# Kernel tuning notes

Hardware: AMD Instinct MI355X
Metric: run time of the kernel (lower is better)

Reference implementation:

```python
import jax, jax.numpy as jnp
import numpy as np

N_NODES = 100000
N_EDGES = 3200000
D_IN = 256
HID = 256
N_CLASSES = 40


def setup_inputs() -> dict:
    key = jax.random.key(0)
    k1, k2, k3, k4 = jax.random.split(key, 4)
    x = jax.random.normal(k1, (N_NODES, D_IN), dtype=jnp.float32)
    edge_index = jax.random.randint(k2, (2, N_EDGES), 0, N_NODES, dtype=jnp.int64)
    W1 = jax.random.normal(k3, (D_IN, HID), dtype=jnp.float32) * (1.0 / np.sqrt(D_IN))
    b1 = jnp.zeros((HID,), dtype=jnp.float32)
    W2 = jax.random.normal(k4, (HID, N_CLASSES), dtype=jnp.float32) * (1.0 / np.sqrt(HID))
    b2 = jnp.zeros((N_CLASSES,), dtype=jnp.float32)
    return {"x": x, "edge_index": edge_index, "W1": W1, "b1": b1, "W2": W2, "b2": b2}


def reference(x, edge_index, W1, b1, W2, b2):
    N = x.shape[0]
    loops = jnp.arange(N, dtype=edge_index.dtype)
    # gcn_norm: add self-loops, symmetric normalization D^-1/2 (A+I) D^-1/2
    src = jnp.concatenate([edge_index[0], loops])  # [E+N]
    dst = jnp.concatenate([edge_index[1], loops])
    ew = jnp.ones(src.shape[0], dtype=x.dtype)
    deg = jax.ops.segment_sum(ew, dst, num_segments=N)  # degree at target nodes
    dinv = jnp.where(deg > 0, jax.lax.rsqrt(deg), 0.0).astype(x.dtype)
    norm = dinv[src] * dinv[dst]  # [E+N]

    def propagate(h):
        # out[dst] += norm * h[src]  (SpMM via gather + segment scatter-add)
        return jax.ops.segment_sum(norm[:, None] * h[src], dst, num_segments=N)

    h = propagate(x) @ W1 + b1   # SGConv k=1 + Linear
    h = jax.nn.relu(h)
    h = propagate(h) @ W2 + b2
    return jax.nn.log_softmax(h, axis=1)
```

## Files before the change

kernel.cpp:

```cpp
#include <hip/hip_runtime.h>
#include <hip/hip_bf16.h>

#define N_NODES 100000
#define N_EDGES 3200000
#define D_IN 256
#define HID 256
#define NC 40
#define NBUCK 391
#define CHUNK 8192
#define BIN1_BLOCKS ((N_EDGES + CHUNK - 1) / CHUNK)
#define BCAP 16384
#define NPADE (NBUCK * BCAP)

typedef unsigned short u16;
typedef unsigned int u32;
typedef __attribute__((ext_vector_type(8))) short bf16x8;
typedef __attribute__((ext_vector_type(4))) float f32x4;
typedef __attribute__((ext_vector_type(2))) float f32x2;

static __device__ __forceinline__ float bf2f(u16 u) {
  union { unsigned int i; float f; } c; c.i = ((unsigned int)u) << 16; return c.f;
}
static __device__ __forceinline__ u16 f2bf(float f) {
  union { float f; unsigned int i; } c; c.f = f;
  unsigned int x = c.i;
  x += 0x7fffu + ((x >> 16) & 1u);
  return (u16)(x >> 16);
}

__global__ void k_zero(int* __restrict__ gcur) {
  int i = blockIdx.x * 256 + threadIdx.x;
  if (i < NBUCK) gcur[i] = i * BCAP;
}

__global__ __launch_bounds__(256) void k_bin1(const int* __restrict__ ei,
    int* __restrict__ gcur, u32* __restrict__ binned) {
  __shared__ int cnt[NBUCK];
  __shared__ int base[NBUCK];
  int t = threadIdx.x;
  int e0 = blockIdx.x * CHUNK;
  for (int j = t; j < NBUCK; j += 256) cnt[j] = 0;
  __syncthreads();
  for (int j = 0; j < CHUNK / 256; ++j) {
    int e = e0 + j * 256 + t;
    if (e < N_EDGES) {
      unsigned d = (unsigned)ei[N_EDGES + e];
      if (d < N_NODES) atomicAdd(&cnt[d >> 8], 1);
    }
  }
  __syncthreads();
  for (int j = t; j < NBUCK; j += 256)
    base[j] = cnt[j] ? atomicAdd(&gcur[j], cnt[j]) : 0;
  __syncthreads();
  for (int j = 0; j < CHUNK / 256; ++j) {
    int e = e0 + j * 256 + t;
    if (e < N_EDGES) {
      unsigned s = (unsigned)ei[e];
      unsigned d = (unsigned)ei[N_EDGES + e];
      if (s < N_NODES && d < N_NODES) {
        int b = d >> 8;
        int pos = atomicAdd(&base[b], 1);
        if ((unsigned)pos < NPADE)
          binned[pos] = ((d & 255u) << 17) | s;
      }
    }
  }
}

__global__ __launch_bounds__(256) void k_bin2(const u32* __restrict__ binned,
    const int* __restrict__ gcur, int* __restrict__ rp, int* __restrict__ re,
    float* __restrict__ dinv, int* __restrict__ ed) {
  __shared__ int cnt[256];
  __shared__ int s[256];
  __shared__ int cur[256];
  int b = blockIdx.x, t = threadIdx.x;
  int start = b * BCAP, end = gcur[b];
  cnt[t] = 0;
  __syncthreads();
  for (int i = start + t; i < end; i += 256)
    atomicAdd(&cnt[binned[i] >> 17], 1);
  __syncthreads();
  int v = cnt[t];
  s[t] = v;
  __syncthreads();
  for (int off = 1; off < 256; off <<= 1) {
    int add = (t >= off) ? s[t - off] : 0;
    __syncthreads();
    s[t] += add;
    __syncthreads();
  }
  int excl = s[t] - v;
  int n = b * 256 + t;
  if (n < N_NODES) {
    rp[n] = start + excl;
    re[n] = start + excl + v;
    dinv[n] = rsqrtf((float)v + 1.0f);
  }
  cur[t] = start + excl;
  __syncthreads();
  for (int i = start + t; i < end; i += 256) {
    u32 rec = binned[i];
    int pos = atomicAdd(&cur[rec >> 17], 1);
    if ((unsigned)pos < NPADE) ed[pos] = (int)(rec & 0x1FFFFu);
  }
}

__global__ void k_w1t(const float* __restrict__ W1, u16* __restrict__ w1t) {
  int n = blockIdx.x, k = threadIdx.x;
  w1t[n * 256 + k] = f2bf(W1[k * 256 + n]);
}
__global__ void k_w2t(const float* __restrict__ W2, u16* __restrict__ w2t) {
  int n = blockIdx.x, k = threadIdx.x;
  w2t[n * 256 + k] = (n < NC) ? f2bf(W2[k * NC + n]) : (u16)0;
}

__global__ __launch_bounds__(256) void k_gemm1(const float* __restrict__ x,
    const u16* __restrict__ w1t, const float* __restrict__ dinv,
    unsigned char* __restrict__ y) {
  __shared__ char smem[20480];
  short* sA = (short*)smem;
  short* sB = (short*)(smem + 10240);
  float* sdinv = (float*)(smem + 18432);
  int tid = threadIdx.x;
  int wave = tid >> 6, lane = tid & 63;
  int lq = lane >> 4, lr = lane & 15;
  int wm = (wave >> 1) * 64, wn = (wave & 1) * 64;
  int row0 = blockIdx.y * 128;
  int col0 = blockIdx.x * 128;
  int sr = tid >> 1;
  int sh = (tid & 1) * 16;
  int arow = row0 + sr;
  bool aval = arow < N_NODES;
  const float* axf = x + (size_t)arow * 256 + sh;
  const u16* bx = w1t + (size_t)(col0 + sr) * 256 + sh;
  f32x4 acc[4][4] = {};
  for (int k0 = 0; k0 < 256; k0 += 32) {
    float4 f0 = {}, f1 = {}, f2 = {}, f3 = {};
    if (aval) {
      f0 = *(const float4*)(axf + k0);
      f1 = *(const float4*)(axf + k0 + 4);
      f2 = *(const float4*)(axf + k0 + 8);
      f3 = *(const float4*)(axf + k0 + 12);
    }
    uint4 vb0 = *(const uint4*)(bx + k0);
    uint4 vb1 = *(const uint4*)(bx + k0 + 8);
    uint4 pa0, pa1;
    pa0.x = (u32)f2bf(f0.x) | ((u32)f2bf(f0.y) << 16);
    pa0.y = (u32)f2bf(f0.z) | ((u32)f2bf(f0.w) << 16);
    pa0.z = (u32)f2bf(f1.x) | ((u32)f2bf(f1.y) << 16);
    pa0.w = (u32)f2bf(f1.z) | ((u32)f2bf(f1.w) << 16);
    pa1.x = (u32)f2bf(f2.x) | ((u32)f2bf(f2.y) << 16);
    pa1.y = (u32)f2bf(f2.z) | ((u32)f2bf(f2.w) << 16);
    pa1.z = (u32)f2bf(f3.x) | ((u32)f2bf(f3.y) << 16);
    pa1.w = (u32)f2bf(f3.z) | ((u32)f2bf(f3.w) << 16);
    __syncthreads();
    *(uint4*)&sA[sr * 40 + sh] = pa0;
    *(uint4*)&sA[sr * 40 + sh + 8] = pa1;
    *(uint4*)&sB[sr * 40 + sh] = vb0;
    *(uint4*)&sB[sr * 40 + sh + 8] = vb1;
    __syncthreads();
    bf16x8 af[4], bfr[4];
#pragma unroll
    for (int mt = 0; mt < 4; ++mt)
      af[mt] = *(const bf16x8*)&sA[(wm + mt * 16 + lr) * 40 + lq * 8];
#pragma unroll
    for (int nt = 0; nt < 4; ++nt)
      bfr[nt] = *(const bf16x8*)&sB[(wn + nt * 16 + lr) * 40 + lq * 8];
#pragma unroll
    for (int mt = 0; mt < 4; ++mt)
#pragma unroll
      for (int nt = 0; nt < 4; ++nt)
        acc[mt][nt] = __builtin_amdgcn_mfma_f32_16x16x32_bf16(
            af[mt], bfr[nt], acc[mt][nt], 0, 0, 0);
  }
  __syncthreads();
  if (tid < 128) {
    int rr = row0 + tid;
    sdinv[tid] = (rr < N_NODES) ? dinv[rr] : 0.f;
  }
  __syncthreads();
#pragma unroll
  for (int mt = 0; mt < 4; ++mt)
#pragma unroll
    for (int nt = 0; nt < 4; ++nt) {
      int c = wn + nt * 16 + lr;
#pragma unroll
      for (int i = 0; i < 4; ++i) {
        int r = wm + mt * 16 + lq * 4 + i;
        float sv = sdinv[r] * acc[mt][nt][i];
        int pk = __builtin_amdgcn_cvt_pk_fp8_f32(sv, sv, 0, false);
        smem[r * 144 + c] = (char)(pk & 0xFF);
      }
    }
  __syncthreads();
  if (aval) {
    unsigned char* dst = y + (size_t)arow * 256 + col0 + (tid & 1) * 64;
    const char* srcp = smem + sr * 144 + (tid & 1) * 64;
#pragma unroll
    for (int j = 0; j < 4; ++j)
      ((uint4*)dst)[j] = *(const uint4*)(srcp + j * 16);
  }
}

#define ACC8(U) do { \
    acc[0] += __builtin_amdgcn_cvt_pk_f32_fp8((U).x, false); \
    acc[1] += __builtin_amdgcn_cvt_pk_f32_fp8((U).x, true);  \
    acc[2] += __builtin_amdgcn_cvt_pk_f32_fp8((U).y, false); \
    acc[3] += __builtin_amdgcn_cvt_pk_f32_fp8((U).y, true);  \
    acc[4] += __builtin_amdgcn_cvt_pk_f32_fp8((U).z, false); \
    acc[5] += __builtin_amdgcn_cvt_pk_f32_fp8((U).z, true);  \
    acc[6] += __builtin_amdgcn_cvt_pk_f32_fp8((U).w, false); \
    acc[7] += __builtin_amdgcn_cvt_pk_f32_fp8((U).w, true);  \
  } while (0)

__global__ __launch_bounds__(256) void k_spmm1(const uint4* __restrict__ y16,
    const int* __restrict__ ed, const int* __restrict__ rp,
    const int* __restrict__ re, const float* __restrict__ dinv,
    const float* __restrict__ b1, u16* __restrict__ h1) {
  int lane = threadIdx.x & 63;
  int row = (blockIdx.x << 2) + (threadIdx.x >> 6);
  int g = lane >> 4, p = lane & 15;
  float di = dinv[row];
  uint4 sv = y16[(size_t)row * 16 + p];
  f32x2 acc[8];
  f32x2 z2 = {0.f, 0.f};
  if (g == 0) {
    acc[0] = __builtin_amdgcn_cvt_pk_f32_fp8(sv.x, false);
    acc[1] = __builtin_amdgcn_cvt_pk_f32_fp8(sv.x, true);
    acc[2] = __builtin_amdgcn_cvt_pk_f32_fp8(sv.y, false);
    acc[3] = __builtin_amdgcn_cvt_pk_f32_fp8(sv.y, true);
    acc[4] = __builtin_amdgcn_cvt_pk_f32_fp8(sv.z, false);
    acc[5] = __builtin_amdgcn_cvt_pk_f32_fp8(sv.z, true);
    acc[6] = __builtin_amdgcn_cvt_pk_f32_fp8(sv.w, false);
    acc[7] = __builtin_amdgcn_cvt_pk_f32_fp8(sv.w, true);
  } else {
#pragma unroll
    for (int i = 0; i < 8; ++i) acc[i] = z2;
  }
  int e = rp[row], e1 = re[row];
  for (; e + 8 <= e1; e += 8) {
    int s0 = ed[e + g];
    int s1 = ed[e + 4 + g];
    uint4 u0 = y16[(size_t)s0 * 16 + p];
    uint4 u1 = y16[(size_t)s1 * 16 + p];
    ACC8(u0);
    ACC8(u1);
  }
  for (; e + 4 <= e1; e += 4) {
    int s0 = ed[e + g];
    uint4 u0 = y16[(size_t)s0 * 16 + p];
    ACC8(u0);
  }
  int rem = e1 - e;
  if (rem > 0) {
    int s0 = ed[e + (g < rem ? g : 0)];
    uint4 u0 = y16[(size_t)s0 * 16 + p];
    if (g < rem) ACC8(u0);
  }
#pragma unroll
  for (int i = 0; i < 8; ++i) {
    acc[i].x += __shfl_xor(acc[i].x, 16);
    acc[i].y += __shfl_xor(acc[i].y, 16);
    acc[i].x += __shfl_xor(acc[i].x, 32);
    acc[i].y += __shfl_xor(acc[i].y, 32);
  }
  if (g == 0) {
    const float4* bb4 = (const float4*)(b1 + p * 16);
    u16 o[16];
#pragma unroll
    for (int i = 0; i < 4; ++i) {
      float4 bb = bb4[i];
      float a0 = fmaxf(di * acc[2 * i].x + bb.x, 0.f);
      float a1 = fmaxf(di * acc[2 * i].y + bb.y, 0.f);
      float a2 = fmaxf(di * acc[2 * i + 1].x + bb.z, 0.f);
      float a3 = fmaxf(di * acc[2 * i + 1].y + bb.w, 0.f);
      o[4 * i + 0] = f2bf(a0);
      o[4 * i + 1] = f2bf(a1);
      o[4 * i + 2] = f2bf(a2);
      o[4 * i + 3] = f2bf(a3);
    }
    u16* dst = h1 + (size_t)row * HID + p * 16;
    *(uint4*)dst = *(const uint4*)&o[0];
    *(uint4*)(dst + 8) = *(const uint4*)&o[8];
  }
}

__global__ __launch_bounds__(256) void k_gemm2(const u16* __restrict__ h1,
    const u16* __restrict__ w2t, const float* __restrict__ dinv,
    u16* __restrict__ zb) {
  __shared__ char smem[16384];
  short* sA = (short*)smem;
  short* sB = (short*)(smem + 10240);
  float* sdinv = (float*)(smem + 14336);
  u16* sC = (u16*)smem;
  int tid = threadIdx.x;
  int wave = tid >> 6, lane = tid & 63;
  int lq = lane >> 4, lr = lane & 15;
  int wm = wave * 32;
  int row0 = blockIdx.x * 128;
  int sr = tid >> 1;
  int sh = (tid & 1) * 16;
  int arow = row0 + sr;
  bool aval = arow < N_NODES;
  const u16* ax = h1 + (size_t)arow * 256 + sh;
  int br = tid >> 1;
  const u16* bx = w2t + (size_t)br * 256 + sh;
  if (tid < 128) {
    int rr = row0 + tid;
    sdinv[tid] = (rr < N_NODES) ? dinv[rr] : 0.f;
  }
  f32x4 acc[2][3] = {};
  for (int k0 = 0; k0 < 256; k0 += 32) {
    uint4 a0 = {}, a1 = {};
    if (aval) {
      a0 = *(const uint4*)(ax + k0);
      a1 = *(const uint4*)(ax + k0 + 8);
    }
    uint4 b0 = {}, b1v = {};
    if (tid < 96) {
      b0 = *(const uint4*)(bx + k0);
      b1v = *(const uint4*)(bx + k0 + 8);
    }
    __syncthreads();
    *(uint4*)&sA[sr * 40 + sh] = a0;
    *(uint4*)&sA[sr * 40 + sh + 8] = a1;
    if (tid < 96) {
      *(uint4*)&sB[br * 40 + sh] = b0;
      *(uint4*)&sB[br * 40 + sh + 8] = b1v;
    }
    __syncthreads();
    bf16x8 af[2], bfr[3];
#pragma unroll
    for (int mt = 0; mt < 2; ++mt)
      af[mt] = *(const bf16x8*)&sA[(wm + mt * 16 + lr) * 40 + lq * 8];
#pragma unroll
    for (int nt = 0; nt < 3; ++nt)
      bfr[nt] = *(const bf16x8*)&sB[(nt * 16 + lr) * 40 + lq * 8];
#pragma unroll
    for (int mt = 0; mt < 2; ++mt)
#pragma unroll
      for (int nt = 0; nt < 3; ++nt)
        acc[mt][nt] = __builtin_amdgcn_mfma_f32_16x16x32_bf16(
            af[mt], bfr[nt], acc[mt][nt], 0, 0, 0);
  }
  __syncthreads();
#pragma unroll
  for (int mt = 0; mt < 2; ++mt)
#pragma unroll
    for (int nt = 0; nt < 3; ++nt) {
      int c = nt * 16 + lr;
#pragma unroll
      for (int i = 0; i < 4; ++i) {
        int r = wm + mt * 16 + lq * 4 + i;
        sC[r * 56 + c] = f2bf(sdinv[r] * acc[mt][nt][i]);
      }
    }
  __syncthreads();
  if (tid < 128) {
    int orow = row0 + tid;
    if (orow < N_NODES) {
      u16* dst = zb + (size_t)orow * NC;
#pragma unroll
      for (int j = 0; j < 5; ++j)
        ((uint4*)dst)[j] = *(const uint4*)&sC[tid * 56 + j * 8];
    }
  }
}

__global__ __launch_bounds__(256) void k_spmm2(const u16* __restrict__ zb,
    const int* __restrict__ ed, const int* __restrict__ rp,
    const int* __restrict__ re, const float* __restrict__ dinv,
    const float* __restrict__ b2, float* __restrict__ out) {
  int lane = threadIdx.x & 63;
  int row = (blockIdx.x << 2) + (threadIdx.x >> 6);
  int col = (lane < NC) ? lane : 0;
  float di = dinv[row];
  float acc = bf2f(zb[(size_t)row * NC + col]);
  int e = rp[row], e1 = re[row];
  for (; e + 8 <= e1; e += 8) {
    int s0 = ed[e], s1 = ed[e + 1], s2 = ed[e + 2], s3 = ed[e + 3];
    int s4 = ed[e + 4], s5 = ed[e + 5], s6 = ed[e + 6], s7 = ed[e + 7];
    u16 z0 = zb[(size_t)s0 * NC + col];
    u16 z1 = zb[(size_t)s1 * NC + col];
    u16 z2 = zb[(size_t)s2 * NC + col];
    u16 z3 = zb[(size_t)s3 * NC + col];
    u16 z4 = zb[(size_t)s4 * NC + col];
    u16 z5 = zb[(size_t)s5 * NC + col];
    u16 z6 = zb[(size_t)s6 * NC + col];
    u16 z7 = zb[(size_t)s7 * NC + col];
    acc += ((bf2f(z0) + bf2f(z1)) + (bf2f(z2) + bf2f(z3))) +
           ((bf2f(z4) + bf2f(z5)) + (bf2f(z6) + bf2f(z7)));
  }
  for (; e < e1; ++e)
    acc += bf2f(zb[(size_t)ed[e] * NC + col]);
  acc = di * acc + b2[col];
  float mv = (lane < NC) ? acc : -3.0e38f;
  for (int off = 32; off > 0; off >>= 1) mv = fmaxf(mv, __shfl_xor(mv, off));
  float ex = (lane < NC) ? expf(acc - mv) : 0.f;
  float sum = ex;
  for (int off = 32; off > 0; off >>= 1) sum += __shfl_xor(sum, off);
  float res = acc - mv - logf(sum);
  if (lane < NC) out[(size_t)row * NC + lane] = res;
}

extern "C" void kernel_launch(void* const* d_in, const int* in_sizes, int n_in,
                              void* d_out, int out_size, void* d_ws, size_t ws_size,
                              hipStream_t stream) {
  const float* x  = (const float*)d_in[0];
  const int*   ei = (const int*)d_in[1];
  const float* W1 = (const float*)d_in[2];
  const float* b1 = (const float*)d_in[3];
  const float* W2 = (const float*)d_in[4];
  const float* b2 = (const float*)d_in[5];
  float* out = (float*)d_out;

  char* ws = (char*)d_ws;
  size_t off = 0;
  auto alloc = [&](size_t bytes) {
    char* p = ws + off;
    off = (off + bytes + 255) & ~(size_t)255;
    return p;
  };
  int*   gcur   = (int*)  alloc((size_t)NBUCK * 4);
  int*   rp     = (int*)  alloc((size_t)N_NODES * 4);
  int*   re     = (int*)  alloc((size_t)N_NODES * 4);
  float* dinv   = (float*)alloc((size_t)N_NODES * 4);
  u32*   binned = (u32*)  alloc((size_t)NPADE * 4);
  int*   ed     = (int*)  alloc((size_t)NPADE * 4);
  unsigned char* y = (unsigned char*)alloc((size_t)N_NODES * 256);
  u16*   w1t    = (u16*)  alloc((size_t)256 * 256 * 2);
  u16*   w2t    = (u16*)  alloc((size_t)48 * 256 * 2);
  u16*   h1     = (u16*)  alloc((size_t)N_NODES * HID * 2);
  u16*   zb     = (u16*)  alloc((size_t)N_NODES * NC * 2);

  k_zero<<<2, 256, 0, stream>>>(gcur);
  k_bin1<<<BIN1_BLOCKS, 256, 0, stream>>>(ei, gcur, binned);
  k_bin2<<<NBUCK, 256, 0, stream>>>(binned, gcur, rp, re, dinv, ed);
  k_w1t<<<256, 256, 0, stream>>>(W1, w1t);
  k_w2t<<<48, 256, 0, stream>>>(W2, w2t);
  k_gemm1<<<dim3(2, (N_NODES + 127) / 128), 256, 0, stream>>>(x, w1t, dinv, y);
  k_spmm1<<<N_NODES / 4, 256, 0, stream>>>((const uint4*)y, ed, rp, re, dinv, b1, h1);
  k_gemm2<<<(N_NODES + 127) / 128, 256, 0, stream>>>(h1, w2t, dinv, zb);
  k_spmm2<<<N_NODES / 4, 256, 0, stream>>>(zb, ed, rp, re, dinv, b2, out);
}
```

Baseline: 514.8 us.

## Pad second-layer features to 64 and gather 8 edges per wave with uint4 loads

The second-layer intermediate is now stored padded to 64 bf16 columns (128-byte rows). The second SpMM splits each wave into 8 groups of 8 lanes, so each group handles a different edge and fetches a whole row segment with 16-byte loads instead of per-lane 2-byte loads. Partial sums are reduced across groups with shuffles, and log-softmax is computed over 8 values per lane. This cuts the number of memory instructions and the serial edge-loop length, at the cost of extra padded bytes written and read, plus cross-lane reductions.

```diff
diff --git a/kernel.cpp b/kernel.cpp
--- a/kernel.cpp
+++ b/kernel.cpp
@@ -287,7 +287,7 @@
 
 __global__ __launch_bounds__(256) void k_gemm2(const u16* __restrict__ h1,
     const u16* __restrict__ w2t, const float* __restrict__ dinv,
-    u16* __restrict__ zb) {
+    u16* __restrict__ zbp) {
   __shared__ char smem[16384];
   short* sA = (short*)smem;
   short* sB = (short*)(smem + 10240);
@@ -359,48 +359,121 @@
   if (tid < 128) {
     int orow = row0 + tid;
     if (orow < N_NODES) {
-      u16* dst = zb + (size_t)orow * NC;
-#pragma unroll
-      for (int j = 0; j < 5; ++j)
+      u16* dst = zbp + (size_t)orow * 64;
+#pragma unroll
+      for (int j = 0; j < 6; ++j)
         ((uint4*)dst)[j] = *(const uint4*)&sC[tid * 56 + j * 8];
-    }
-  }
-}
-
-__global__ __launch_bounds__(256) void k_spmm2(const u16* __restrict__ zb,
+      uint4 z = {};
+      ((uint4*)dst)[6] = z;
+      ((uint4*)dst)[7] = z;
+    }
+  }
+}
+
+#define ZACC(U) do { \
+    acc[0] += __uint_as_float((U).x << 16); \
+    acc[1] += __uint_as_float((U).x & 0xFFFF0000u); \
+    acc[2] += __uint_as_float((U).y << 16); \
+    acc[3] += __uint_as_float((U).y & 0xFFFF0000u); \
+    acc[4] += __uint_as_float((U).z << 16); \
+    acc[5] += __uint_as_float((U).z & 0xFFFF0000u); \
+    acc[6] += __uint_as_float((U).w << 16); \
+    acc[7] += __uint_as_float((U).w & 0xFFFF0000u); \
+  } while (0)
+
+__global__ __launch_bounds__(256) void k_spmm2(const uint4* __restrict__ zb4,
     const int* __restrict__ ed, const int* __restrict__ rp,
     const int* __restrict__ re, const float* __restrict__ dinv,
     const float* __restrict__ b2, float* __restrict__ out) {
   int lane = threadIdx.x & 63;
   int row = (blockIdx.x << 2) + (threadIdx.x >> 6);
-  int col = (lane < NC) ? lane : 0;
+  int g = lane >> 3, p = lane & 7;
   float di = dinv[row];
-  float acc = bf2f(zb[(size_t)row * NC + col]);
+  float acc[8];
+  uint4 sv = zb4[(size_t)row * 8 + p];
+  if (g == 0) {
+    acc[0] = __uint_as_float(sv.x << 16);
+    acc[1] = __uint_as_float(sv.x & 0xFFFF0000u);
+    acc[2] = __uint_as_float(sv.y << 16);
+    acc[3] = __uint_as_float(sv.y & 0xFFFF0000u);
+    acc[4] = __uint_as_float(sv.z << 16);
+    acc[5] = __uint_as_float(sv.z & 0xFFFF0000u);
+    acc[6] = __uint_as_float(sv.w << 16);
+    acc[7] = __uint_as_float(sv.w & 0xFFFF0000u);
+  } else {
+#pragma unroll
+    for (int i = 0; i < 8; ++i) acc[i] = 0.f;
+  }
   int e = rp[row], e1 = re[row];
+  for (; e + 16 <= e1; e += 16) {
+    int s0 = ed[e + g];
+    int s1 = ed[e + 8 + g];
+    uint4 u0 = zb4[(size_t)s0 * 8 + p];
+    uint4 u1 = zb4[(size_t)s1 * 8 + p];
+    ZACC(u0);
+    ZACC(u1);
+  }
   for (; e + 8 <= e1; e += 8) {
-    int s0 = ed[e], s1 = ed[e + 1], s2 = ed[e + 2], s3 = ed[e + 3];
-    int s4 = ed[e + 4], s5 = ed[e + 5], s6 = ed[e + 6], s7 = ed[e + 7];
-    u16 z0 = zb[(size_t)s0 * NC + col];
-    u16 z1 = zb[(size_t)s1 * NC + col];
-    u16 z2 = zb[(size_t)s2 * NC + col];
-    u16 z3 = zb[(size_t)s3 * NC + col];
-    u16 z4 = zb[(size_t)s4 * NC + col];
-    u16 z5 = zb[(size_t)s5 * NC + col];
-    u16 z6 = zb[(size_t)s6 * NC + col];
-    u16 z7 = zb[(size_t)s7 * NC + col];
-    acc += ((bf2f(z0) + bf2f(z1)) + (bf2f(z2) + bf2f(z3))) +
-           ((bf2f(z4) + bf2f(z5)) + (bf2f(z6) + bf2f(z7)));
-  }
-  for (; e < e1; ++e)
-    acc += bf2f(zb[(size_t)ed[e] * NC + col]);
-  acc = di * acc + b2[col];
-  float mv = (lane < NC) ? acc : -3.0e38f;
-  for (int off = 32; off > 0; off >>= 1) mv = fmaxf(mv, __shfl_xor(mv, off));
-  float ex = (lane < NC) ? expf(acc - mv) : 0.f;
-  float sum = ex;
-  for (int off = 32; off > 0; off >>= 1) sum += __shfl_xor(sum, off);
-  float res = acc - mv - logf(sum);
-  if (lane < NC) out[(size_t)row * NC + lane] = res;
+    int s0 = ed[e + g];
+    uint4 u0 = zb4[(size_t)s0 * 8 + p];
+    ZACC(u0);
+  }
+  int rem = e1 - e;
+  if (g < rem) {
+    int s0 = ed[e + g];
+    uint4 u0 = zb4[(size_t)s0 * 8 + p];
+    ZACC(u0);
+  }
+#pragma unroll
+  for (int i = 0; i < 8; ++i) {
+    acc[i] += __shfl_xor(acc[i], 8);
+    acc[i] += __shfl_xor(acc[i], 16);
+    acc[i] += __shfl_xor(acc[i], 32);
+  }
+  bool valid = p < 5;
+  float val[8];
+  if (valid) {
+    float4 bb0 = *(const float4*)(b2 + p * 8);
+    float4 bb1 = *(const float4*)(b2 + p * 8 + 4);
+    val[0] = di * acc[0] + bb0.x;
+    val[1] = di * acc[1] + bb0.y;
+    val[2] = di * acc[2] + bb0.z;
+    val[3] = di * acc[3] + bb0.w;
+    val[4] = di * acc[4] + bb1.x;
+    val[5] = di * acc[5] + bb1.y;
+    val[6] = di * acc[6] + bb1.z;
+    val[7] = di * acc[7] + bb1.w;
+  } else {
+#pragma unroll
+    for (int i = 0; i < 8; ++i) val[i] = 0.f;
+  }
+  float mv = -3.0e38f;
+  if (valid) {
+#pragma unroll
+    for (int i = 0; i < 8; ++i) mv = fmaxf(mv, val[i]);
+  }
+  mv = fmaxf(mv, __shfl_xor(mv, 1));
+  mv = fmaxf(mv, __shfl_xor(mv, 2));
+  mv = fmaxf(mv, __shfl_xor(mv, 4));
+  float sum = 0.f;
+  if (valid) {
+#pragma unroll
+    for (int i = 0; i < 8; ++i) sum += expf(val[i] - mv);
+  }
+  sum += __shfl_xor(sum, 1);
+  sum += __shfl_xor(sum, 2);
+  sum += __shfl_xor(sum, 4);
+  float ls = logf(sum);
+  if (g == 0 && valid) {
+    float4 o0, o1;
+    o0.x = val[0] - mv - ls; o0.y = val[1] - mv - ls;
+    o0.z = val[2] - mv - ls; o0.w = val[3] - mv - ls;
+    o1.x = val[4] - mv - ls; o1.y = val[5] - mv - ls;
+    o1.z = val[6] - mv - ls; o1.w = val[7] - mv - ls;
+    float* dst = out + (size_t)row * NC + p * 8;
+    *(float4*)dst = o0;
+    *(float4*)(dst + 4) = o1;
+  }
 }
 
 extern "C" void kernel_launch(void* const* d_in, const int* in_sizes, int n_in,
@@ -431,7 +504,7 @@
   u16*   w1t    = (u16*)  alloc((size_t)256 * 256 * 2);
   u16*   w2t    = (u16*)  alloc((size_t)48 * 256 * 2);
   u16*   h1     = (u16*)  alloc((size_t)N_NODES * HID * 2);
-  u16*   zb     = (u16*)  alloc((size_t)N_NODES * NC * 2);
+  u16*   zbp    = (u16*)  alloc((size_t)N_NODES * 64 * 2);
 
   k_zero<<<2, 256, 0, stream>>>(gcur);
   k_bin1<<<BIN1_BLOCKS, 256, 0, stream>>>(ei, gcur, binned);
@@ -440,6 +513,6 @@
   k_w2t<<<48, 256, 0, stream>>>(W2, w2t);
   k_gemm1<<<dim3(2, (N_NODES + 127) / 128), 256, 0, stream>>>(x, w1t, dinv, y);
   k_spmm1<<<N_NODES / 4, 256, 0, stream>>>((const uint4*)y, ed, rp, re, dinv, b1, h1);
-  k_gemm2<<<(N_NODES + 127) / 128, 256, 0, stream>>>(h1, w2t, dinv, zb);
-  k_spmm2<<<N_NODES / 4, 256, 0, stream>>>(zb, ed, rp, re, dinv, b2, out);
-}
+  k_gemm2<<<(N_NODES + 127) / 128, 256, 0, stream>>>(h1, w2t, dinv, zbp);
+  k_spmm2<<<N_NODES / 4, 256, 0, stream>>>((const uint4*)zbp, ed, rp, re, dinv, b2, out);
+}
```

New measurement: 494.6 us. -3.9%, faster.
